# Performance work log

Measured on AMD Instinct MI355X. Metric: run time of the kernel, lower is better.

The kernel has to match this reference:

```python
import jax, jax.numpy as jnp
import numpy as np

N_NODES = 100000


def gcn_conv(x, W, b, src, dst, n):
    # PyG GCNConv: add self-loops, symmetric deg^-1/2 normalization,
    # transform then gather/scatter-add aggregate.
    loop = jnp.arange(n, dtype=src.dtype)
    s = jnp.concatenate([src, loop])
    d = jnp.concatenate([dst, loop])
    deg = jax.ops.segment_sum(jnp.ones_like(d, dtype=x.dtype), d, num_segments=n)
    dinv = jnp.where(deg > 0, 1.0 / jnp.sqrt(deg), 0.0)
    norm = dinv[s] * dinv[d]                      # [E+N]
    h = x @ W                                     # [N, out]
    msgs = h[s] * norm[:, None]                   # gather + scale
    out = jax.ops.segment_sum(msgs, d, num_segments=n)  # scatter-add
    return out + b


def setup_inputs() -> dict:
    key = jax.random.key(0)
    k1, k2, k3, k4 = jax.random.split(key, 4)
    F_in, H, D = 128, 16, 128
    x = jax.random.normal(k1, (N_NODES, F_in), dtype=jnp.float32)
    edge_index = jax.random.randint(k2, (2, 1600000), 0, N_NODES, dtype=jnp.int64)
    W1 = jax.random.normal(k3, (F_in, H), dtype=jnp.float32) / np.sqrt(F_in)
    b1 = jnp.zeros((H,), dtype=jnp.float32)
    W2 = jax.random.normal(k4, (H, D), dtype=jnp.float32) / np.sqrt(H)
    b2 = jnp.zeros((D,), dtype=jnp.float32)
    return {"x": x, "edge_index": edge_index, "W1": W1, "b1": b1, "W2": W2, "b2": b2}


def reference(x, edge_index, W1, b1, W2, b2):
    src, dst = edge_index[0], edge_index[1]
    n = x.shape[0]
    h = jax.nn.relu(gcn_conv(x, W1, b1, src, dst, n))
    out = jax.nn.relu(gcn_conv(h, W2, b2, src, dst, n))
    return out
```

## Files before the change

kernel.cpp:

```cpp
#include <hip/hip_runtime.h>
#include <hip/hip_fp16.h>
#include <stdint.h>

#define F_IN  128
#define HID   16
#define F_OUT 128
#define NBK   512
#define NBLK  512
#define BCAP  4096
#define CHUNK_MAX 4096
#define GT2_NODES 128
#define T1N   64
#define AGP   24
#define WP    136

typedef _Float16 f16;
typedef f16 f16x4 __attribute__((ext_vector_type(4)));
typedef f16 f16x8 __attribute__((ext_vector_type(8)));
typedef float f32x4 __attribute__((ext_vector_type(4)));

__device__ __forceinline__ int bucket_of(int d, int N) {
    return (int)(((long long)d * NBK) / N);
}
__device__ __forceinline__ int bucket_lo(int b, int N) {
    return (int)(((long long)b * N + NBK - 1) / NBK);
}

__global__ void __launch_bounds__(256) k_partf(
        const int* __restrict__ ei, int* __restrict__ bcur,
        uint32_t* __restrict__ pairs, int E, int N) {
    __shared__ int lh[NBK], lofs[NBK], lcur[NBK], gbase[NBK], lnlo[NBK];
    __shared__ int loff[256];
    __shared__ uint32_t spairs[CHUNK_MAX];
    __shared__ uint16_t sbkt[CHUNK_MAX];

    int blk = blockIdx.x, t = threadIdx.x;
    int Cr = (E + NBLK - 1) / NBLK;
    int C  = (Cr + 15) & ~15;
    int e0 = blk * C; if (e0 > E) e0 = E;
    int e1 = e0 + C;  if (e1 > E) e1 = E;
    int ecnt = e1 - e0;

    for (int i = t; i < NBK; i += 256) { lh[i] = 0; lnlo[i] = bucket_lo(i, N); }
    __syncthreads();

    int4 es4[4], ed4[4];
    bool evec = ((E & 3) == 0);
#pragma unroll
    for (int j = 0; j < 4; ++j) {
        int e = e0 + (j * 256 + t) * 4;
        if (evec && e + 4 <= e1) {
            es4[j] = *(const int4*)(ei + e);
            ed4[j] = *(const int4*)(ei + E + e);
        } else {
            int* s = (int*)&es4[j];
            int* d = (int*)&ed4[j];
#pragma unroll
            for (int q = 0; q < 4; ++q) {
                int ee = e + q;
                bool ok = (ee < e1);
                s[q] = ok ? ei[ee] : -1;
                d[q] = ok ? ei[E + ee] : 0;
            }
        }
    }
    const int* esv = (const int*)es4;
    const int* edv = (const int*)ed4;
    int eb[16];
#pragma unroll
    for (int k = 0; k < 16; ++k) {
        if (esv[k] >= 0) {
            eb[k] = bucket_of(edv[k], N);
            atomicAdd(&lh[eb[k]], 1);
        } else eb[k] = -1;
    }
    __syncthreads();

    int a0 = lh[2 * t], a1 = lh[2 * t + 1];
    int s2 = a0 + a1;
    loff[t] = s2;
    __syncthreads();
    for (int o = 1; o < 256; o <<= 1) {
        int a = (t >= o) ? loff[t - o] : 0;
        __syncthreads();
        loff[t] += a;
        __syncthreads();
    }
    int excl = loff[t] - s2;
    lofs[2 * t]     = excl;
    lofs[2 * t + 1] = excl + a0;
    lcur[2 * t]     = excl;
    lcur[2 * t + 1] = excl + a0;
    __syncthreads();

    for (int w = 0; w < NBK; w += 256) {
        int i = (t + w + blk) & (NBK - 1);
        int h = lh[i];
        gbase[i] = h ? atomicAdd(&bcur[i], h) : 0;
    }

#pragma unroll
    for (int k = 0; k < 16; ++k) {
        if (eb[k] >= 0) {
            int b = eb[k];
            int idx = atomicAdd(&lcur[b], 1);
            spairs[idx] = ((uint32_t)esv[k] << 10) | (uint32_t)(edv[k] - lnlo[b]);
            sbkt[idx]   = (uint16_t)b;
        }
    }
    __syncthreads();

    for (int i = t; i < ecnt; i += 256) {
        int b = sbkt[i];
        int pos = gbase[b] + (i - lofs[b]);
        if (pos < BCAP)
            pairs[(size_t)b * BCAP + pos] = spairs[i];
    }
}

__global__ void __launch_bounds__(256) k_csr2(
        const uint32_t* __restrict__ pairs, const int* __restrict__ bcur,
        int2* __restrict__ meta, float* __restrict__ dinv,
        int* __restrict__ srcs, int N) {
    __shared__ uint32_t sp[BCAP];
    __shared__ int lcnt[256];
    __shared__ int loff[256];
    __shared__ int lcur[256];
    int b = blockIdx.x, t = threadIdx.x;
    int base = b * BCAP;
    int ec = bcur[b]; if (ec > BCAP) ec = BCAP;
    int nlo = bucket_lo(b, N);
    int nhi = bucket_lo(b + 1, N); if (nhi > N) nhi = N;
    int nn = nhi - nlo;
    lcnt[t] = 0;
    __syncthreads();
    int ec4 = (ec + 3) >> 2;
    for (int i = t; i < ec4; i += 256) {
        uint4 v = *(const uint4*)(pairs + base + i * 4);
        *(uint4*)&sp[i * 4] = v;
        int lim = ec - i * 4;
        if (lim > 0) atomicAdd(&lcnt[v.x & 1023u], 1);
        if (lim > 1) atomicAdd(&lcnt[v.y & 1023u], 1);
        if (lim > 2) atomicAdd(&lcnt[v.z & 1023u], 1);
        if (lim > 3) atomicAdd(&lcnt[v.w & 1023u], 1);
    }
    __syncthreads();
    int v = lcnt[t];
    int pv = (v + 3) & ~3;
    loff[t] = pv;
    __syncthreads();
    for (int o = 1; o < 256; o <<= 1) {
        int a = (t >= o) ? loff[t - o] : 0;
        __syncthreads();
        loff[t] += a;
        __syncthreads();
    }
    if (t < nn) {
        int gs = base + (loff[t] - pv);
        meta[nlo + t] = make_int2(gs, v);
        dinv[nlo + t] = rsqrtf((float)(v + 1));
        lcur[t]       = gs;
    }
    __syncthreads();
    for (int e = t; e < ec; e += 256) {
        uint32_t p = sp[e];
        int pos = atomicAdd(&lcur[p & 1023u], 1);
        srcs[pos] = (int)(p >> 10);
    }
}

__global__ void __launch_bounds__(256) k_transform1(
        const float* __restrict__ x, const float* __restrict__ W1,
        const float* __restrict__ dinv, __half* __restrict__ g1, int n) {
    __shared__ __align__(16) f16 sWh[HID * WP];
    __shared__ __align__(16) f16 sWl[HID * WP];
    int t = threadIdx.x;
    int node0 = blockIdx.x * T1N;
    for (int i = t; i < F_IN * HID; i += 256) {
        int k = i >> 4, f = i & 15;
        float wv = W1[i];
        f16 h = (f16)wv;
        sWh[f * WP + k] = h;
        sWl[f * WP + k] = (f16)(wv - (float)h);
    }
    __syncthreads();
    int lane = t & 63, wave = t >> 6;
    int mcol = lane & 15, kg = lane >> 4;
    int nrow = node0 + wave * 16 + mcol;
    int crow = nrow < n ? nrow : (n - 1);
    const float* xr = x + (size_t)crow * F_IN;
    f32x4 acc = {0.f, 0.f, 0.f, 0.f};
#pragma unroll
    for (int ks = 0; ks < 4; ++ks) {
        int k0 = ks * 32 + kg * 8;
        float4 v0 = *(const float4*)(xr + k0);
        float4 v1 = *(const float4*)(xr + k0 + 4);
        float va[8] = {v0.x, v0.y, v0.z, v0.w, v1.x, v1.y, v1.z, v1.w};
        f16x8 ah, al;
#pragma unroll
        for (int q = 0; q < 8; ++q) {
            f16 h = (f16)va[q];
            ah[q] = h;
            al[q] = (f16)(va[q] - (float)h);
        }
        f16x8 bh = *(const f16x8*)&sWh[mcol * WP + k0];
        f16x8 bl = *(const f16x8*)&sWl[mcol * WP + k0];
        acc = __builtin_amdgcn_mfma_f32_16x16x32_f16(ah, bh, acc, 0, 0, 0);
        acc = __builtin_amdgcn_mfma_f32_16x16x32_f16(al, bh, acc, 0, 0, 0);
        acc = __builtin_amdgcn_mfma_f32_16x16x32_f16(ah, bl, acc, 0, 0, 0);
    }
#pragma unroll
    for (int r = 0; r < 4; ++r) {
        int node = node0 + wave * 16 + kg * 4 + r;
        if (node < n) {
            float di = dinv[node];
            g1[(size_t)node * HID + mcol] = __float2half(di * acc[r]);
        }
    }
}

__device__ __forceinline__ void add_h8(float* __restrict__ acc, const __half* __restrict__ ptr) {
    uint4 u = *(const uint4*)ptr;
    const __half2* h = (const __half2*)&u;
#pragma unroll
    for (int q = 0; q < 4; ++q) {
        float2 f = __half22float2(h[q]);
        acc[2 * q]     += f.x;
        acc[2 * q + 1] += f.y;
    }
}

__device__ __forceinline__ void gather_acc(
        float* __restrict__ acc, int node, int p,
        const __half* __restrict__ g, const int* __restrict__ srcs,
        int rs, int deg) {
    {
        uint4 u = *(const uint4*)(g + (size_t)node * HID + p * 8);
        const __half2* h = (const __half2*)&u;
#pragma unroll
        for (int q = 0; q < 4; ++q) {
            float2 f = __half22float2(h[q]);
            acc[2 * q] = f.x; acc[2 * q + 1] = f.y;
        }
    }
    int j = 0;
    for (; j + 8 <= deg; j += 8) {
        int4 ia = *(const int4*)(srcs + rs + j);
        int4 ib = *(const int4*)(srcs + rs + j + 4);
        add_h8(acc, g + (size_t)ia.x * HID + p * 8);
        add_h8(acc, g + (size_t)ia.y * HID + p * 8);
        add_h8(acc, g + (size_t)ia.z * HID + p * 8);
        add_h8(acc, g + (size_t)ia.w * HID + p * 8);
        add_h8(acc, g + (size_t)ib.x * HID + p * 8);
        add_h8(acc, g + (size_t)ib.y * HID + p * 8);
        add_h8(acc, g + (size_t)ib.z * HID + p * 8);
        add_h8(acc, g + (size_t)ib.w * HID + p * 8);
    }
    if (j + 4 <= deg) {
        int4 ia = *(const int4*)(srcs + rs + j);
        add_h8(acc, g + (size_t)ia.x * HID + p * 8);
        add_h8(acc, g + (size_t)ia.y * HID + p * 8);
        add_h8(acc, g + (size_t)ia.z * HID + p * 8);
        add_h8(acc, g + (size_t)ia.w * HID + p * 8);
        j += 4;
    }
    for (; j < deg; ++j)
        add_h8(acc, g + (size_t)srcs[rs + j] * HID + p * 8);
}

__global__ void __launch_bounds__(256) k_gather1(
        const __half* __restrict__ g, const int* __restrict__ srcs,
        const int2* __restrict__ meta, const float* __restrict__ dinv,
        const float* __restrict__ b1, __half* __restrict__ outb, int n) {
    int tt = blockIdx.x * 256 + threadIdx.x;
    int node = tt >> 1;
    int p = tt & 1;
    if (node >= n) return;
    int2 m = meta[node];
    float acc[8];
    gather_acc(acc, node, p, g, srcs, m.x, m.y);
    float di = dinv[node];
#pragma unroll
    for (int i = 0; i < 8; ++i)
        acc[i] = di * fmaxf(di * acc[i] + b1[p * 8 + i], 0.0f);
    uint4 o;
    __half2* oh = (__half2*)&o;
#pragma unroll
    for (int q = 0; q < 4; ++q)
        oh[q] = __floats2half2_rn(acc[2 * q], acc[2 * q + 1]);
    *(uint4*)(outb + (size_t)node * HID + p * 8) = o;
}

__global__ void __launch_bounds__(256) k_gather_t2(
        const __half* __restrict__ g, const int* __restrict__ srcs,
        const int2* __restrict__ meta, const float* __restrict__ dinv,
        const float* __restrict__ W2, const float* __restrict__ b2,
        float* __restrict__ out, int n) {
    __shared__ __half sAgg[GT2_NODES * AGP];
    __shared__ float  sdv[GT2_NODES];
    int t = threadIdx.x;
    int node0 = blockIdx.x * GT2_NODES;

    {
        int nl = t >> 1, p = t & 1;
        int node = node0 + nl;
        if (node < n) {
            if (p == 0) sdv[nl] = dinv[node];
            int2 m = meta[node];
            float acc[8];
            gather_acc(acc, node, p, g, srcs, m.x, m.y);
            uint4 o;
            __half2* oh = (__half2*)&o;
#pragma unroll
            for (int q = 0; q < 4; ++q)
                oh[q] = __floats2half2_rn(acc[2 * q], acc[2 * q + 1]);
            *(uint4*)&sAgg[nl * AGP + p * 8] = o;
        }
    }
    __syncthreads();

    int lane = t & 63, wave = t >> 6;
    int fcol = lane & 15, kg = lane >> 4;
    int k0 = kg * 4;
    f16x4 bh[8], bl[8];
    float b2v[8];
#pragma unroll
    for (int nt = 0; nt < 8; ++nt) {
        b2v[nt] = b2[nt * 16 + fcol];
#pragma unroll
        for (int j = 0; j < 4; ++j) {
            float wv = W2[(k0 + j) * F_OUT + nt * 16 + fcol];
            f16 h = (f16)wv;
            bh[nt][j] = h;
            bl[nt][j] = (f16)(wv - (float)h);
        }
    }
    const f16* sA = (const f16*)sAgg;
    f16x4 aA = *(const f16x4*)&sA[(wave * 32 + fcol) * AGP + k0];
    f16x4 aB = *(const f16x4*)&sA[(wave * 32 + 16 + fcol) * AGP + k0];
    f32x4 zero = {0.f, 0.f, 0.f, 0.f};
    f32x4 acc[2][8];
#pragma unroll
    for (int mt = 0; mt < 2; ++mt)
#pragma unroll
        for (int nt = 0; nt < 8; ++nt)
            acc[mt][nt] = zero;
#pragma unroll
    for (int nt = 0; nt < 8; ++nt) {
        acc[0][nt] = __builtin_amdgcn_mfma_f32_16x16x16f16(aA, bh[nt], acc[0][nt], 0, 0, 0);
        acc[0][nt] = __builtin_amdgcn_mfma_f32_16x16x16f16(aA, bl[nt], acc[0][nt], 0, 0, 0);
        acc[1][nt] = __builtin_amdgcn_mfma_f32_16x16x16f16(aB, bh[nt], acc[1][nt], 0, 0, 0);
        acc[1][nt] = __builtin_amdgcn_mfma_f32_16x16x16f16(aB, bl[nt], acc[1][nt], 0, 0, 0);
    }
#pragma unroll
    for (int mt = 0; mt < 2; ++mt) {
#pragma unroll
        for (int r = 0; r < 4; ++r) {
            int ln = wave * 32 + mt * 16 + kg * 4 + r;
            int node = node0 + ln;
            if (node < n) {
                float dv = sdv[ln];
#pragma unroll
                for (int nt = 0; nt < 8; ++nt)
                    out[(size_t)node * F_OUT + nt * 16 + fcol] =
                        fmaxf(dv * acc[mt][nt][r] + b2v[nt], 0.f);
            }
        }
    }
}

extern "C" void kernel_launch(void* const* d_in, const int* in_sizes, int n_in,
                              void* d_out, int out_size, void* d_ws, size_t ws_size,
                              hipStream_t stream) {
    const float* x  = (const float*)d_in[0];
    const int*   ei = (const int*)d_in[1];
    const float* W1 = (const float*)d_in[2];
    const float* b1 = (const float*)d_in[3];
    const float* W2 = (const float*)d_in[4];
    const float* b2 = (const float*)d_in[5];
    float* out = (float*)d_out;

    const int N = in_sizes[0] / F_IN;
    const int E = in_sizes[1] / 2;

    float* dinv      = (float*)d_ws;
    int2*  meta      = (int2*)(dinv + N);
    int*   bcur      = (int*)(meta + N);
    int*   srcs      = bcur + NBK;
    uint32_t* pairs  = (uint32_t*)(srcs + (size_t)NBK * BCAP);
    __half* bufA     = (__half*)(pairs + (size_t)NBK * BCAP);
    __half* bufB     = bufA + (size_t)N * HID;

    hipMemsetAsync(bcur, 0, NBK * sizeof(int), stream);
    k_partf<<<NBLK, 256, 0, stream>>>(ei, bcur, pairs, E, N);
    k_csr2 <<<NBK, 256, 0, stream>>>(pairs, bcur, meta, dinv, srcs, N);
    k_transform1<<<(N + T1N - 1) / T1N, 256, 0, stream>>>(x, W1, dinv, bufA, N);
    k_gather1<<<((size_t)N * 2 + 255) / 256, 256, 0, stream>>>(
        bufA, srcs, meta, dinv, b1, bufB, N);
    k_gather_t2<<<(N + GT2_NODES - 1) / GT2_NODES, 256, 0, stream>>>(
        bufB, srcs, meta, dinv, W2, b2, out, N);
}
```

Baseline: 186.0 us.

## Process nodes in degree-sorted order within buckets to balance gather warps

During CSR build, each bucket counting-sorts its nodes by in-degree (capped at 255) and writes a permutation array. Both gather kernels then visit nodes through this permutation, so lanes of a wavefront handle nodes of similar degree. This is meant to cut divergence and the idle lanes left by uneven gather loop lengths. The cost is an extra scan and scatter in k_csr2, an indirect node lookup, and scattered output writes (the final 128-float rows of k_gather_t2 are no longer contiguous per block).

```diff
diff --git a/kernel.cpp b/kernel.cpp
--- a/kernel.cpp
+++ b/kernel.cpp
@@ -121,7 +121,7 @@
 __global__ void __launch_bounds__(256) k_csr2(
         const uint32_t* __restrict__ pairs, const int* __restrict__ bcur,
         int2* __restrict__ meta, float* __restrict__ dinv,
-        int* __restrict__ srcs, int N) {
+        int* __restrict__ srcs, int* __restrict__ perm, int N) {
     __shared__ uint32_t sp[BCAP];
     __shared__ int lcnt[256];
     __shared__ int loff[256];
@@ -166,6 +166,28 @@
         uint32_t p = sp[e];
         int pos = atomicAdd(&lcur[p & 1023u], 1);
         srcs[pos] = (int)(p >> 10);
+    }
+    __syncthreads();
+
+    int bin = v < 255 ? v : 255;
+    lcnt[t] = 0;
+    __syncthreads();
+    if (t < nn) atomicAdd(&lcnt[bin], 1);
+    __syncthreads();
+    int bv = lcnt[t];
+    loff[t] = bv;
+    __syncthreads();
+    for (int o = 1; o < 256; o <<= 1) {
+        int a = (t >= o) ? loff[t - o] : 0;
+        __syncthreads();
+        loff[t] += a;
+        __syncthreads();
+    }
+    lcur[t] = loff[t] - bv;
+    __syncthreads();
+    if (t < nn) {
+        int r = atomicAdd(&lcur[bin], 1);
+        perm[nlo + r] = nlo + t;
     }
 }
 
@@ -271,11 +293,13 @@
 __global__ void __launch_bounds__(256) k_gather1(
         const __half* __restrict__ g, const int* __restrict__ srcs,
         const int2* __restrict__ meta, const float* __restrict__ dinv,
-        const float* __restrict__ b1, __half* __restrict__ outb, int n) {
+        const float* __restrict__ b1, const int* __restrict__ perm,
+        __half* __restrict__ outb, int n) {
     int tt = blockIdx.x * 256 + threadIdx.x;
-    int node = tt >> 1;
+    int ni = tt >> 1;
     int p = tt & 1;
-    if (node >= n) return;
+    if (ni >= n) return;
+    int node = perm[ni];
     int2 m = meta[node];
     float acc[8];
     gather_acc(acc, node, p, g, srcs, m.x, m.y);
@@ -295,17 +319,19 @@
         const __half* __restrict__ g, const int* __restrict__ srcs,
         const int2* __restrict__ meta, const float* __restrict__ dinv,
         const float* __restrict__ W2, const float* __restrict__ b2,
-        float* __restrict__ out, int n) {
+        const int* __restrict__ perm, float* __restrict__ out, int n) {
     __shared__ __half sAgg[GT2_NODES * AGP];
     __shared__ float  sdv[GT2_NODES];
+    __shared__ int    snode[GT2_NODES];
     int t = threadIdx.x;
     int node0 = blockIdx.x * GT2_NODES;
 
     {
         int nl = t >> 1, p = t & 1;
-        int node = node0 + nl;
-        if (node < n) {
-            if (p == 0) sdv[nl] = dinv[node];
+        int ni = node0 + nl;
+        if (ni < n) {
+            int node = perm[ni];
+            if (p == 0) { sdv[nl] = dinv[node]; snode[nl] = node; }
             int2 m = meta[node];
             float acc[8];
             gather_acc(acc, node, p, g, srcs, m.x, m.y);
@@ -357,8 +383,8 @@
 #pragma unroll
         for (int r = 0; r < 4; ++r) {
             int ln = wave * 32 + mt * 16 + kg * 4 + r;
-            int node = node0 + ln;
-            if (node < n) {
+            if (node0 + ln < n) {
+                int node = snode[ln];
                 float dv = sdv[ln];
 #pragma unroll
                 for (int nt = 0; nt < 8; ++nt)
@@ -385,7 +411,8 @@
 
     float* dinv      = (float*)d_ws;
     int2*  meta      = (int2*)(dinv + N);
-    int*   bcur      = (int*)(meta + N);
+    int*   perm      = (int*)(meta + N);
+    int*   bcur      = perm + N;
     int*   srcs      = bcur + NBK;
     uint32_t* pairs  = (uint32_t*)(srcs + (size_t)NBK * BCAP);
     __half* bufA     = (__half*)(pairs + (size_t)NBK * BCAP);
@@ -393,10 +420,10 @@
 
     hipMemsetAsync(bcur, 0, NBK * sizeof(int), stream);
     k_partf<<<NBLK, 256, 0, stream>>>(ei, bcur, pairs, E, N);
-    k_csr2 <<<NBK, 256, 0, stream>>>(pairs, bcur, meta, dinv, srcs, N);
+    k_csr2 <<<NBK, 256, 0, stream>>>(pairs, bcur, meta, dinv, srcs, perm, N);
     k_transform1<<<(N + T1N - 1) / T1N, 256, 0, stream>>>(x, W1, dinv, bufA, N);
     k_gather1<<<((size_t)N * 2 + 255) / 256, 256, 0, stream>>>(
-        bufA, srcs, meta, dinv, b1, bufB, N);
+        bufA, srcs, meta, dinv, b1, perm, bufB, N);
     k_gather_t2<<<(N + GT2_NODES - 1) / GT2_NODES, 256, 0, stream>>>(
-        bufB, srcs, meta, dinv, W2, b2, out, N);
-}
+        bufB, srcs, meta, dinv, W2, b2, perm, out, N);
+}
```

New measurement: 192.6 us. 1.04x slower.

## Split each node's neighbor gather across two thread pairs with shuffle reduction

Applied to the files above, without the earlier changes.

The two gather kernels now assign four threads per node instead of two, with each pair handling half of the node's neighbor list. The partial sums are combined with a cross-lane shuffle. The second-layer kernel processes 64 nodes per block so each wave runs one MFMA row tile. This aims to raise memory-level parallelism and shorten the per-thread serial gather chain on the latency-bound random reads, at the cost of twice as many threads, extra shuffles, and less work per block in the MFMA epilogue.

```diff
diff --git a/kernel.cpp b/kernel.cpp
--- a/kernel.cpp
+++ b/kernel.cpp
@@ -9,7 +9,7 @@
 #define NBLK  512
 #define BCAP  4096
 #define CHUNK_MAX 4096
-#define GT2_NODES 128
+#define GT2_NODES 64
 #define T1N   64
 #define AGP   24
 #define WP    136
@@ -230,23 +230,14 @@
     }
 }
 
-__device__ __forceinline__ void gather_acc(
-        float* __restrict__ acc, int node, int p,
+__device__ __forceinline__ void gather_run(
+        float* __restrict__ acc, int p,
         const __half* __restrict__ g, const int* __restrict__ srcs,
-        int rs, int deg) {
-    {
-        uint4 u = *(const uint4*)(g + (size_t)node * HID + p * 8);
-        const __half2* h = (const __half2*)&u;
-#pragma unroll
-        for (int q = 0; q < 4; ++q) {
-            float2 f = __half22float2(h[q]);
-            acc[2 * q] = f.x; acc[2 * q + 1] = f.y;
-        }
-    }
+        int rs0, int cnt) {
     int j = 0;
-    for (; j + 8 <= deg; j += 8) {
-        int4 ia = *(const int4*)(srcs + rs + j);
-        int4 ib = *(const int4*)(srcs + rs + j + 4);
+    for (; j + 8 <= cnt; j += 8) {
+        int4 ia = *(const int4*)(srcs + rs0 + j);
+        int4 ib = *(const int4*)(srcs + rs0 + j + 4);
         add_h8(acc, g + (size_t)ia.x * HID + p * 8);
         add_h8(acc, g + (size_t)ia.y * HID + p * 8);
         add_h8(acc, g + (size_t)ia.z * HID + p * 8);
@@ -256,16 +247,41 @@
         add_h8(acc, g + (size_t)ib.z * HID + p * 8);
         add_h8(acc, g + (size_t)ib.w * HID + p * 8);
     }
-    if (j + 4 <= deg) {
-        int4 ia = *(const int4*)(srcs + rs + j);
+    if (j + 4 <= cnt) {
+        int4 ia = *(const int4*)(srcs + rs0 + j);
         add_h8(acc, g + (size_t)ia.x * HID + p * 8);
         add_h8(acc, g + (size_t)ia.y * HID + p * 8);
         add_h8(acc, g + (size_t)ia.z * HID + p * 8);
         add_h8(acc, g + (size_t)ia.w * HID + p * 8);
         j += 4;
     }
-    for (; j < deg; ++j)
-        add_h8(acc, g + (size_t)srcs[rs + j] * HID + p * 8);
+    for (; j < cnt; ++j)
+        add_h8(acc, g + (size_t)srcs[rs0 + j] * HID + p * 8);
+}
+
+__device__ __forceinline__ void gather_acc4(
+        float* __restrict__ acc, int node, int p, int q,
+        const __half* __restrict__ g, const int* __restrict__ srcs,
+        int rs, int deg) {
+    int h = ((deg + 4) >> 3) << 2;
+    if (h > deg) h = deg;
+    if (q == 0) {
+        uint4 u = *(const uint4*)(g + (size_t)node * HID + p * 8);
+        const __half2* hh = (const __half2*)&u;
+#pragma unroll
+        for (int w = 0; w < 4; ++w) {
+            float2 f = __half22float2(hh[w]);
+            acc[2 * w] = f.x; acc[2 * w + 1] = f.y;
+        }
+        gather_run(acc, p, g, srcs, rs, h);
+    } else {
+#pragma unroll
+        for (int w = 0; w < 8; ++w) acc[w] = 0.f;
+        gather_run(acc, p, g, srcs, rs + h, deg - h);
+    }
+#pragma unroll
+    for (int w = 0; w < 8; ++w)
+        acc[w] += __shfl_xor(acc[w], 2, 64);
 }
 
 __global__ void __launch_bounds__(256) k_gather1(
@@ -273,22 +289,25 @@
         const int2* __restrict__ meta, const float* __restrict__ dinv,
         const float* __restrict__ b1, __half* __restrict__ outb, int n) {
     int tt = blockIdx.x * 256 + threadIdx.x;
-    int node = tt >> 1;
+    int node = tt >> 2;
     int p = tt & 1;
+    int q = (tt >> 1) & 1;
     if (node >= n) return;
     int2 m = meta[node];
     float acc[8];
-    gather_acc(acc, node, p, g, srcs, m.x, m.y);
-    float di = dinv[node];
-#pragma unroll
-    for (int i = 0; i < 8; ++i)
-        acc[i] = di * fmaxf(di * acc[i] + b1[p * 8 + i], 0.0f);
-    uint4 o;
-    __half2* oh = (__half2*)&o;
-#pragma unroll
-    for (int q = 0; q < 4; ++q)
-        oh[q] = __floats2half2_rn(acc[2 * q], acc[2 * q + 1]);
-    *(uint4*)(outb + (size_t)node * HID + p * 8) = o;
+    gather_acc4(acc, node, p, q, g, srcs, m.x, m.y);
+    if (q == 0) {
+        float di = dinv[node];
+#pragma unroll
+        for (int i = 0; i < 8; ++i)
+            acc[i] = di * fmaxf(di * acc[i] + b1[p * 8 + i], 0.0f);
+        uint4 o;
+        __half2* oh = (__half2*)&o;
+#pragma unroll
+        for (int w = 0; w < 4; ++w)
+            oh[w] = __floats2half2_rn(acc[2 * w], acc[2 * w + 1]);
+        *(uint4*)(outb + (size_t)node * HID + p * 8) = o;
+    }
 }
 
 __global__ void __launch_bounds__(256) k_gather_t2(
@@ -302,19 +321,21 @@
     int node0 = blockIdx.x * GT2_NODES;
 
     {
-        int nl = t >> 1, p = t & 1;
+        int nl = t >> 2, p = t & 1, q = (t >> 1) & 1;
         int node = node0 + nl;
         if (node < n) {
-            if (p == 0) sdv[nl] = dinv[node];
+            if (t == (nl << 2)) sdv[nl] = dinv[node];
             int2 m = meta[node];
             float acc[8];
-            gather_acc(acc, node, p, g, srcs, m.x, m.y);
-            uint4 o;
-            __half2* oh = (__half2*)&o;
-#pragma unroll
-            for (int q = 0; q < 4; ++q)
-                oh[q] = __floats2half2_rn(acc[2 * q], acc[2 * q + 1]);
-            *(uint4*)&sAgg[nl * AGP + p * 8] = o;
+            gather_acc4(acc, node, p, q, g, srcs, m.x, m.y);
+            if (q == 0) {
+                uint4 o;
+                __half2* oh = (__half2*)&o;
+#pragma unroll
+                for (int w = 0; w < 4; ++w)
+                    oh[w] = __floats2half2_rn(acc[2 * w], acc[2 * w + 1]);
+                *(uint4*)&sAgg[nl * AGP + p * 8] = o;
+            }
         }
     }
     __syncthreads();
@@ -336,35 +357,26 @@
         }
     }
     const f16* sA = (const f16*)sAgg;
-    f16x4 aA = *(const f16x4*)&sA[(wave * 32 + fcol) * AGP + k0];
-    f16x4 aB = *(const f16x4*)&sA[(wave * 32 + 16 + fcol) * AGP + k0];
+    f16x4 aA = *(const f16x4*)&sA[(wave * 16 + fcol) * AGP + k0];
     f32x4 zero = {0.f, 0.f, 0.f, 0.f};
-    f32x4 acc[2][8];
-#pragma unroll
-    for (int mt = 0; mt < 2; ++mt)
-#pragma unroll
-        for (int nt = 0; nt < 8; ++nt)
-            acc[mt][nt] = zero;
+    f32x4 acc[8];
+#pragma unroll
+    for (int nt = 0; nt < 8; ++nt) acc[nt] = zero;
 #pragma unroll
     for (int nt = 0; nt < 8; ++nt) {
-        acc[0][nt] = __builtin_amdgcn_mfma_f32_16x16x16f16(aA, bh[nt], acc[0][nt], 0, 0, 0);
-        acc[0][nt] = __builtin_amdgcn_mfma_f32_16x16x16f16(aA, bl[nt], acc[0][nt], 0, 0, 0);
-        acc[1][nt] = __builtin_amdgcn_mfma_f32_16x16x16f16(aB, bh[nt], acc[1][nt], 0, 0, 0);
-        acc[1][nt] = __builtin_amdgcn_mfma_f32_16x16x16f16(aB, bl[nt], acc[1][nt], 0, 0, 0);
-    }
-#pragma unroll
-    for (int mt = 0; mt < 2; ++mt) {
-#pragma unroll
-        for (int r = 0; r < 4; ++r) {
-            int ln = wave * 32 + mt * 16 + kg * 4 + r;
-            int node = node0 + ln;
-            if (node < n) {
-                float dv = sdv[ln];
-#pragma unroll
-                for (int nt = 0; nt < 8; ++nt)
-                    out[(size_t)node * F_OUT + nt * 16 + fcol] =
-                        fmaxf(dv * acc[mt][nt][r] + b2v[nt], 0.f);
-            }
+        acc[nt] = __builtin_amdgcn_mfma_f32_16x16x16f16(aA, bh[nt], acc[nt], 0, 0, 0);
+        acc[nt] = __builtin_amdgcn_mfma_f32_16x16x16f16(aA, bl[nt], acc[nt], 0, 0, 0);
+    }
+#pragma unroll
+    for (int r = 0; r < 4; ++r) {
+        int ln = wave * 16 + kg * 4 + r;
+        int node = node0 + ln;
+        if (node < n) {
+            float dv = sdv[ln];
+#pragma unroll
+            for (int nt = 0; nt < 8; ++nt)
+                out[(size_t)node * F_OUT + nt * 16 + fcol] =
+                    fmaxf(dv * acc[nt][r] + b2v[nt], 0.f);
         }
     }
 }
@@ -395,7 +407,7 @@
     k_partf<<<NBLK, 256, 0, stream>>>(ei, bcur, pairs, E, N);
     k_csr2 <<<NBK, 256, 0, stream>>>(pairs, bcur, meta, dinv, srcs, N);
     k_transform1<<<(N + T1N - 1) / T1N, 256, 0, stream>>>(x, W1, dinv, bufA, N);
-    k_gather1<<<((size_t)N * 2 + 255) / 256, 256, 0, stream>>>(
+    k_gather1<<<((size_t)N * 4 + 255) / 256, 256, 0, stream>>>(
         bufA, srcs, meta, dinv, b1, bufB, N);
     k_gather_t2<<<(N + GT2_NODES - 1) / GT2_NODES, 256, 0, stream>>>(
         bufB, srcs, meta, dinv, W2, b2, out, N);
```

Result: no change. 189.1 us (+1.7%).
